# Performance work log

Measured on AMD Instinct MI355X. Metric: run time of the kernel, lower is better.

Reference implementation:

```python
import jax, jax.numpy as jnp
import numpy as np

D_MODEL, D_FF, N_EXPERTS, TOP_K = 1024, 4096, 4, 2
B, S = 4, 2048


def setup_inputs() -> dict:
    key = jax.random.key(0)
    ks = jax.random.split(key, 7)
    s_r = 1.0 / np.sqrt(D_MODEL)
    s_f = 1.0 / np.sqrt(D_FF)
    return {
        "x": jax.random.normal(ks[0], (B, S, D_MODEL), dtype=jnp.float32),
        "Wr": jax.random.uniform(ks[1], (D_MODEL, N_EXPERTS), jnp.float32, -s_r, s_r),
        "br": jnp.zeros((N_EXPERTS,), jnp.float32),
        "W1": jax.random.uniform(ks[2], (N_EXPERTS, D_MODEL, D_FF), jnp.float32, -s_r, s_r),
        "b1": jax.random.uniform(ks[3], (N_EXPERTS, D_FF), jnp.float32, -s_r, s_r),
        "W2": jax.random.uniform(ks[4], (N_EXPERTS, D_FF, D_MODEL), jnp.float32, -s_f, s_f),
        "b2": jax.random.uniform(ks[5], (N_EXPERTS, D_MODEL), jnp.float32, -s_f, s_f),
    }


def reference(x, Wr, br, W1, b1, W2, b2):
    # Router: (B,S,E)
    router_logits = jnp.einsum("bsd,de->bse", x, Wr) + br
    router_probs = jax.nn.softmax(router_logits, axis=-1)
    top_k_probs, top_k_idx = jax.lax.top_k(router_probs, TOP_K)  # (B,S,K)
    top_k_probs = top_k_probs / jnp.sum(top_k_probs, axis=-1, keepdims=True)

    # Dense all-experts compute (faithful to original module).
    h = jnp.einsum("bsd,edf->bsef", x, W1) + b1          # (B,S,E,F)
    h = jax.nn.gelu(h, approximate=False)                 # torch nn.GELU (erf)
    expert_out = jnp.einsum("bsef,efd->bsed", h, W2) + b2  # (B,S,E,D)

    # Gather top-k expert outputs and combine with renormalized probs.
    sel = jnp.take_along_axis(expert_out, top_k_idx[..., None], axis=2)  # (B,S,K,D)
    out = jnp.sum(sel * top_k_probs[..., None], axis=2)   # (B,S,D)
    return out
```

## Files before the change

### kernel.cpp

```cpp
#include <hip/hip_runtime.h>
#include <hip/hip_bf16.h>
#include <hip/hip_fp16.h>
#include <stdint.h>

typedef float    f32x4 __attribute__((ext_vector_type(4)));
typedef float    fvec4 __attribute__((ext_vector_type(4)));
typedef _Float16 f16x8 __attribute__((ext_vector_type(8)));

#define D_MODEL 1024
#define D_FF    4096
#define NTOK    8192
#define CAP_ROWS 16896
#define NRB      132

#define OFF_W1  0UL
#define OFF_W2  33554432UL
#define OFF_XG  67108864UL
#define OFF_H   101711872UL
#define OFF_CNT 240123904UL
#define OFF_CUR 240123920UL
#define OFF_OFS 240123936UL
#define OFF_TOK 240124160UL
#define OFF_WGT 240191744UL
#define OFF_E12 240259328UL
#define OFF_W12 240292096UL
#define WS_NEED 240357632UL

__device__ __forceinline__ void gload_lds16(const void* g, void* l) {
  __builtin_amdgcn_global_load_lds(
      (const __attribute__((address_space(1))) unsigned int*)g,
      (__attribute__((address_space(3))) unsigned int*)l, 16, 0, 0);
}

__device__ __forceinline__ float fast_gelu(float v) {
  float v2 = v * v;
  float y2 = v * (2.302118131f + 0.10293924f * v2);
  float t = exp2f(y2);
  return v - v * __builtin_amdgcn_rcpf(1.f + t);
}

__device__ __forceinline__ void wtrans_body(
    const float* __restrict__ in, _Float16* __restrict__ out,
    int K, int N, int e, int n0, int k0, float (*tile)[65]) {
  const float* src = in + (size_t)e * K * N;
  _Float16* dst = out + (size_t)e * K * N;
  int t = threadIdx.x;
  {
    int kk = t >> 2, nc = (t & 3) * 16;
    const float* p = src + (size_t)(k0 + kk) * N + n0 + nc;
#pragma unroll
    for (int j = 0; j < 4; ++j) {
      fvec4 v = *(const fvec4*)(p + j * 4);
      tile[kk][nc + j * 4 + 0] = v[0]; tile[kk][nc + j * 4 + 1] = v[1];
      tile[kk][nc + j * 4 + 2] = v[2]; tile[kk][nc + j * 4 + 3] = v[3];
    }
  }
  __syncthreads();
  {
    int nn = t >> 2, kb = (t & 3) * 16;
    f16x8 o0, o1;
#pragma unroll
    for (int j = 0; j < 8; ++j) o0[j] = (_Float16)tile[kb + j][nn];
#pragma unroll
    for (int j = 0; j < 8; ++j) o1[j] = (_Float16)tile[kb + 8 + j][nn];
    _Float16* q = dst + (size_t)(n0 + nn) * K + k0 + kb;
    *(f16x8*)q = o0;
    *((f16x8*)q + 1) = o1;
  }
}

__global__ __launch_bounds__(256) void rw_k(
    const float* __restrict__ x, const float* __restrict__ Wr,
    const float* __restrict__ br, int* __restrict__ e12,
    float* __restrict__ w12,
    const float* __restrict__ W1, _Float16* __restrict__ W1f) {
  __shared__ float tile[64][65];
  int b = blockIdx.x;
  if (b >= 2048) {
    int bb = b - 2048;
    int n0 = (bb & 63) * 64, k0 = ((bb >> 6) & 15) * 64, e = bb >> 10;
    wtrans_body(W1, W1f, 1024, 4096, e, n0, k0, tile);
    return;
  }
  int wid = threadIdx.x >> 6, lane = threadIdx.x & 63;
  int t = b * 4 + wid;
  const float* xr = x + (size_t)t * D_MODEL;
  float a0 = 0.f, a1 = 0.f, a2 = 0.f, a3 = 0.f;
#pragma unroll
  for (int c = 0; c < 4; ++c) {
    int d0 = c * 256 + lane * 4;
    fvec4 xv = *(const fvec4*)(xr + d0);
#pragma unroll
    for (int j = 0; j < 4; ++j) {
      fvec4 wv = *(const fvec4*)(Wr + (size_t)(d0 + j) * 4);
      a0 += xv[j] * wv[0]; a1 += xv[j] * wv[1];
      a2 += xv[j] * wv[2]; a3 += xv[j] * wv[3];
    }
  }
#pragma unroll
  for (int m = 32; m; m >>= 1) {
    a0 += __shfl_xor(a0, m, 64); a1 += __shfl_xor(a1, m, 64);
    a2 += __shfl_xor(a2, m, 64); a3 += __shfl_xor(a3, m, 64);
  }
  if (lane == 0) {
    float l[4] = {a0 + br[0], a1 + br[1], a2 + br[2], a3 + br[3]};
    int e1 = 0; float m1 = l[0];
#pragma unroll
    for (int e = 1; e < 4; ++e) if (l[e] > m1) { m1 = l[e]; e1 = e; }
    int e2 = -1; float m2 = -1e30f;
#pragma unroll
    for (int e = 0; e < 4; ++e) if (e != e1 && l[e] > m2) { m2 = l[e]; e2 = e; }
    float tt = expf(m2 - m1);
    float w1 = 1.f / (1.f + tt), w2 = tt / (1.f + tt);
    e12[t] = e1 | (e2 << 8);
    w12[2 * t] = w1; w12[2 * t + 1] = w2;
  }
}

__global__ __launch_bounds__(256) void plan_k(
    const int* __restrict__ e12, const float* __restrict__ w12,
    int* __restrict__ counts, int* __restrict__ offs,
    int* __restrict__ tok, float* __restrict__ wgt) {
  __shared__ int ls[4][256];
  __shared__ int lt[4];
  __shared__ int lo[5];
  int tid = threadIdx.x;
  int t0 = tid * 32;
  int pe[32];
  int c0 = 0, c1 = 0, c2 = 0, c3 = 0;
#pragma unroll
  for (int j = 0; j < 32; ++j) {
    int p = e12[t0 + j];
    pe[j] = p;
    int e1 = p & 255, e2 = p >> 8;
    c0 += (e1 == 0) + (e2 == 0);
    c1 += (e1 == 1) + (e2 == 1);
    c2 += (e1 == 2) + (e2 == 2);
    c3 += (e1 == 3) + (e2 == 3);
  }
  ls[0][tid] = c0; ls[1][tid] = c1; ls[2][tid] = c2; ls[3][tid] = c3;
  __syncthreads();
  int wv = tid >> 6, lane = tid & 63;
  {
    int s0 = ls[wv][lane * 4 + 0], s1 = ls[wv][lane * 4 + 1];
    int s2 = ls[wv][lane * 4 + 2], s3 = ls[wv][lane * 4 + 3];
    int s = s0 + s1 + s2 + s3;
    int incl = s;
#pragma unroll
    for (int d = 1; d < 64; d <<= 1) {
      int tsh = __shfl_up(incl, d, 64);
      if (lane >= d) incl += tsh;
    }
    int excl = incl - s;
    ls[wv][lane * 4 + 0] = excl;
    ls[wv][lane * 4 + 1] = excl + s0;
    ls[wv][lane * 4 + 2] = excl + s0 + s1;
    ls[wv][lane * 4 + 3] = excl + s0 + s1 + s2;
    if (lane == 63) lt[wv] = incl;
  }
  __syncthreads();
  if (tid == 0) {
    int o = 0;
#pragma unroll
    for (int e = 0; e < 4; ++e) {
      lo[e] = o; offs[e] = o; counts[e] = lt[e];
      o += (lt[e] + 127) & ~127;
    }
    lo[4] = o; offs[4] = o;
  }
  __syncthreads();
  int b0 = lo[0] + ls[0][tid], b1 = lo[1] + ls[1][tid];
  int b2 = lo[2] + ls[2][tid], b3 = lo[3] + ls[3][tid];
#pragma unroll
  for (int j = 0; j < 32; ++j) {
    int p = pe[j];
    int t = t0 + j;
    int e1 = p & 255, e2 = p >> 8;
    int s1 = (e1 == 0) ? b0 : (e1 == 1) ? b1 : (e1 == 2) ? b2 : b3;
    tok[s1] = t; wgt[s1] = w12[2 * t];
    b0 += (e1 == 0); b1 += (e1 == 1); b2 += (e1 == 2); b3 += (e1 == 3);
    int s2 = (e2 == 0) ? b0 : (e2 == 1) ? b1 : (e2 == 2) ? b2 : b3;
    tok[s2] = t; wgt[s2] = w12[2 * t + 1];
    b0 += (e2 == 0); b1 += (e2 == 1); b2 += (e2 == 2); b3 += (e2 == 3);
  }
}

__global__ __launch_bounds__(256) void gather_k(
    const float* __restrict__ x, const int* __restrict__ offs,
    const int* __restrict__ counts, const int* __restrict__ tok,
    _Float16* __restrict__ Xg) {
  int row = blockIdx.x * 2 + (threadIdx.x >> 7);
  int tid = threadIdx.x & 127;
  if (row >= offs[4]) return;
  int e = 0;
  while (e < 3 && row >= offs[e + 1]) ++e;
  f16x8 o;
  if (row < offs[e] + counts[e]) {
    int t = tok[row];
    const float* src = x + (size_t)t * D_MODEL + tid * 8;
    fvec4 v0 = *(const fvec4*)src;
    fvec4 v1 = *(const fvec4*)(src + 4);
#pragma unroll
    for (int j = 0; j < 4; ++j) { o[j] = (_Float16)v0[j]; o[4 + j] = (_Float16)v1[j]; }
  } else {
#pragma unroll
    for (int j = 0; j < 8; ++j) o[j] = (_Float16)0.f;
  }
  *(f16x8*)(Xg + (size_t)row * D_MODEL + tid * 8) = o;
}

__device__ __forceinline__ f16x8 lds_frag(const char* base, int row, int kbyte) {
  return *(const f16x8*)(base + row * 128 + (kbyte ^ ((row & 7) << 4)));
}

__global__ __launch_bounds__(256, 2) void gemm1x_k(
    const _Float16* __restrict__ A, const _Float16* __restrict__ B,
    const float* __restrict__ bias, const int* __restrict__ offs,
    const int* __restrict__ counts, _Float16* __restrict__ outH,
    const float* __restrict__ W2, _Float16* __restrict__ W2f,
    float* __restrict__ outz) {
  __shared__ char lds[49152];
  int bid = blockIdx.x;
  if (bid >= 6208) {
    int b2 = bid - 6208;
    fvec4 z = {0.f, 0.f, 0.f, 0.f};
#pragma unroll
    for (int j = 0; j < 4; ++j)
      *(fvec4*)(outz + (size_t)b2 * 4096 + j * 1024 + threadIdx.x * 4) = z;
    return;
  }
  if (bid >= 2112) {
    int bb = bid - 2112;
    int n0 = (bb & 15) * 64, k0 = ((bb >> 4) & 63) * 64, e = bb >> 10;
    wtrans_body(W2, W2f, 4096, 1024, e, n0, k0, (float(*)[65])lds);
    return;
  }
  int wg = (bid & 7) * 264 + (bid >> 3);
  int col = wg & 15, row = wg >> 4;
  int rowBase = row * 128;
  if (rowBase >= offs[4]) return;
  int e = 0;
  while (e < 3 && rowBase >= offs[e + 1]) ++e;
  if (rowBase >= offs[e] + counts[e]) return;
  int colBase = col * 256;

  int tid = threadIdx.x, wid = tid >> 6, lane = tid & 63;
  int wr = wid >> 1, wc = wid & 1;
  int ln = lane & 15;
  int srow = lane >> 3;
  int kx = (lane & 7) ^ srow;
  const _Float16* Abase = A + (size_t)rowBase * 1024 + kx * 8;
  const _Float16* Bbase = B + (size_t)e * D_FF * 1024 + (size_t)colBase * 1024 + kx * 8;
  char* ldsA = lds;
  char* ldsB = lds + 16384;

  f32x4 acc[4][8];
  f32x4 zero = {0.f, 0.f, 0.f, 0.f};
#pragma unroll
  for (int m = 0; m < 4; ++m)
#pragma unroll
    for (int n = 0; n < 8; ++n) acc[m][n] = zero;

  for (int k0 = 0; k0 < 1024; k0 += 64) {
#pragma unroll
    for (int i = 0; i < 4; ++i) {
      int chunk = wid * 4 + i;
      gload_lds16(Abase + (size_t)(chunk * 8 + srow) * 1024 + k0, ldsA + chunk * 1024);
    }
#pragma unroll
    for (int i = 0; i < 8; ++i) {
      int chunk = wid * 8 + i;
      gload_lds16(Bbase + (size_t)(chunk * 8 + srow) * 1024 + k0, ldsB + chunk * 1024);
    }
    __syncthreads();
#pragma unroll
    for (int kk = 0; kk < 2; ++kk) {
      int kbyte = kk * 64 + (lane >> 4) * 16;
      f16x8 af[4], bf[8];
#pragma unroll
      for (int m = 0; m < 4; ++m)
        af[m] = lds_frag(ldsA, wr * 64 + m * 16 + ln, kbyte);
#pragma unroll
      for (int n = 0; n < 8; ++n)
        bf[n] = lds_frag(ldsB, wc * 128 + n * 16 + ln, kbyte);
#pragma unroll
      for (int m = 0; m < 4; ++m)
#pragma unroll
        for (int n = 0; n < 8; ++n)
          acc[m][n] = __builtin_amdgcn_mfma_f32_16x16x32_f16(af[m], bf[n], acc[m][n], 0, 0, 0);
    }
    __syncthreads();
  }

  int col0 = colBase + wc * 128 + ln;
  float bv[8];
#pragma unroll
  for (int n = 0; n < 8; ++n) bv[n] = bias[(size_t)e * D_FF + col0 + n * 16];
#pragma unroll
  for (int m = 0; m < 4; ++m) {
    int rbase = rowBase + wr * 64 + m * 16 + (lane >> 4) * 4;
#pragma unroll
    for (int j = 0; j < 4; ++j) {
      size_t ro = (size_t)(rbase + j) * D_FF;
#pragma unroll
      for (int n = 0; n < 8; ++n) {
        float v = fast_gelu(acc[m][n][j] + bv[n]);
        outH[ro + col0 + n * 16] = (_Float16)v;
      }
    }
  }
}

__global__ __launch_bounds__(256, 3) void gemm2_k(
    const _Float16* __restrict__ A, const _Float16* __restrict__ B,
    const float* __restrict__ bias, const int* __restrict__ offs,
    const int* __restrict__ counts, const int* __restrict__ tok,
    const float* __restrict__ wgt, float* __restrict__ outF) {
  __shared__ char lds[32768];
  int bid = blockIdx.x;
  int wg = (bid & 7) * 264 + (bid >> 3);
  int col = wg & 7, kz = (wg >> 3) & 1, row = wg >> 4;
  int rowBase = row * 128;
  if (rowBase >= offs[4]) return;
  int e = 0;
  while (e < 3 && rowBase >= offs[e + 1]) ++e;
  int eoff = offs[e], cnt = counts[e];
  if (rowBase >= eoff + cnt) return;
  int colBase = col * 128;
  int kbase = kz * 2048;

  int tid = threadIdx.x, wid = tid >> 6, lane = tid & 63;
  int wr = wid >> 1, wc = wid & 1;
  int ln = lane & 15;
  int srow = lane >> 3;
  int kx = (lane & 7) ^ srow;
  const _Float16* Abase = A + (size_t)rowBase * 4096 + kx * 8;
  const _Float16* Bbase = B + (size_t)e * D_MODEL * 4096 + (size_t)colBase * 4096 + kx * 8;
  char* ldsA = lds;
  char* ldsB = lds + 16384;

  f32x4 acc[4][4];
  f32x4 zero = {0.f, 0.f, 0.f, 0.f};
#pragma unroll
  for (int m = 0; m < 4; ++m)
#pragma unroll
    for (int n = 0; n < 4; ++n) acc[m][n] = zero;

  for (int k0 = kbase; k0 < kbase + 2048; k0 += 64) {
#pragma unroll
    for (int i = 0; i < 4; ++i) {
      int chunk = wid * 4 + i;
      gload_lds16(Abase + (size_t)(chunk * 8 + srow) * 4096 + k0, ldsA + chunk * 1024);
      gload_lds16(Bbase + (size_t)(chunk * 8 + srow) * 4096 + k0, ldsB + chunk * 1024);
    }
    __syncthreads();
#pragma unroll
    for (int kk = 0; kk < 2; ++kk) {
      int kbyte = kk * 64 + (lane >> 4) * 16;
      f16x8 af[4], bf[4];
#pragma unroll
      for (int m = 0; m < 4; ++m)
        af[m] = lds_frag(ldsA, wr * 64 + m * 16 + ln, kbyte);
#pragma unroll
      for (int n = 0; n < 4; ++n)
        bf[n] = lds_frag(ldsB, wc * 64 + n * 16 + ln, kbyte);
#pragma unroll
      for (int m = 0; m < 4; ++m)
#pragma unroll
        for (int n = 0; n < 4; ++n)
          acc[m][n] = __builtin_amdgcn_mfma_f32_16x16x32_f16(af[m], bf[n], acc[m][n], 0, 0, 0);
    }
    __syncthreads();
  }

  int col0 = colBase + wc * 64 + ln;
  float bv[4];
#pragma unroll
  for (int n = 0; n < 4; ++n)
    bv[n] = (kz == 0) ? bias[(size_t)e * D_MODEL + col0 + n * 16] : 0.f;
#pragma unroll
  for (int m = 0; m < 4; ++m) {
    int rbase = rowBase + wr * 64 + m * 16 + (lane >> 4) * 4;
#pragma unroll
    for (int j = 0; j < 4; ++j) {
      int grow = rbase + j;
      if (grow - eoff < cnt) {
        int t = tok[grow];
        float w = wgt[grow];
        size_t o = (size_t)t * D_MODEL + col0;
#pragma unroll
        for (int n = 0; n < 4; ++n)
          atomicAdd(&outF[o + n * 16], w * (acc[m][n][j] + bv[n]));
      }
    }
  }
}

extern "C" void kernel_launch(void* const* d_in, const int* in_sizes, int n_in,
                              void* d_out, int out_size, void* d_ws, size_t ws_size,
                              hipStream_t stream) {
  const float* x  = (const float*)d_in[0];
  const float* Wr = (const float*)d_in[1];
  const float* br = (const float*)d_in[2];
  const float* W1 = (const float*)d_in[3];
  const float* b1 = (const float*)d_in[4];
  const float* W2 = (const float*)d_in[5];
  const float* b2 = (const float*)d_in[6];
  float* out = (float*)d_out;
  char* ws = (char*)d_ws;
  if (ws_size < WS_NEED) return;

  _Float16* W1f = (_Float16*)(ws + OFF_W1);
  _Float16* W2f = (_Float16*)(ws + OFF_W2);
  _Float16* Xg  = (_Float16*)(ws + OFF_XG);
  _Float16* H   = (_Float16*)(ws + OFF_H);
  int*   counts = (int*)(ws + OFF_CNT);
  int*   offs   = (int*)(ws + OFF_OFS);
  int*   tok    = (int*)(ws + OFF_TOK);
  float* wgt    = (float*)(ws + OFF_WGT);
  int*   e12    = (int*)(ws + OFF_E12);
  float* w12    = (float*)(ws + OFF_W12);

  rw_k<<<6144, 256, 0, stream>>>(x, Wr, br, e12, w12, W1, W1f);
  plan_k<<<1, 256, 0, stream>>>(e12, w12, counts, offs, tok, wgt);
  gather_k<<<8448, 256, 0, stream>>>(x, offs, counts, tok, Xg);
  gemm1x_k<<<8256, 256, 0, stream>>>(Xg, W1f, b1, offs, counts, H, W2, W2f, out);
  gemm2_k<<<NRB * 16, 256, 0, stream>>>(H, W2f, b2, offs, counts, tok, wgt, out);
}
```

Measured before the change: 473.8 us.

## Replace split-K atomic scatter in GEMM2 with per-slot fp16 output and combine kernel

```diff
diff --git a/kernel.cpp b/kernel.cpp
--- a/kernel.cpp
+++ b/kernel.cpp
@@ -69,21 +69,12 @@
   }
 }
 
-__global__ __launch_bounds__(256) void rw_k(
+__global__ __launch_bounds__(256) void router_k(
     const float* __restrict__ x, const float* __restrict__ Wr,
     const float* __restrict__ br, int* __restrict__ e12,
-    float* __restrict__ w12,
-    const float* __restrict__ W1, _Float16* __restrict__ W1f) {
-  __shared__ float tile[64][65];
-  int b = blockIdx.x;
-  if (b >= 2048) {
-    int bb = b - 2048;
-    int n0 = (bb & 63) * 64, k0 = ((bb >> 6) & 15) * 64, e = bb >> 10;
-    wtrans_body(W1, W1f, 1024, 4096, e, n0, k0, tile);
-    return;
-  }
+    float* __restrict__ w12) {
   int wid = threadIdx.x >> 6, lane = threadIdx.x & 63;
-  int t = b * 4 + wid;
+  int t = blockIdx.x * 4 + wid;
   const float* xr = x + (size_t)t * D_MODEL;
   float a0 = 0.f, a1 = 0.f, a2 = 0.f, a3 = 0.f;
 #pragma unroll
@@ -118,9 +109,9 @@
 }
 
 __global__ __launch_bounds__(256) void plan_k(
-    const int* __restrict__ e12, const float* __restrict__ w12,
+    int* __restrict__ e12, const float* __restrict__ w12,
     int* __restrict__ counts, int* __restrict__ offs,
-    int* __restrict__ tok, float* __restrict__ wgt) {
+    int* __restrict__ tok) {
   __shared__ int ls[4][256];
   __shared__ int lt[4];
   __shared__ int lo[5];
@@ -177,19 +168,29 @@
     int t = t0 + j;
     int e1 = p & 255, e2 = p >> 8;
     int s1 = (e1 == 0) ? b0 : (e1 == 1) ? b1 : (e1 == 2) ? b2 : b3;
-    tok[s1] = t; wgt[s1] = w12[2 * t];
+    tok[s1] = t;
     b0 += (e1 == 0); b1 += (e1 == 1); b2 += (e1 == 2); b3 += (e1 == 3);
     int s2 = (e2 == 0) ? b0 : (e2 == 1) ? b1 : (e2 == 2) ? b2 : b3;
-    tok[s2] = t; wgt[s2] = w12[2 * t + 1];
+    tok[s2] = t;
     b0 += (e2 == 0); b1 += (e2 == 1); b2 += (e2 == 2); b3 += (e2 == 3);
-  }
-}
-
-__global__ __launch_bounds__(256) void gather_k(
+    e12[t] = s1 | (s2 << 16);
+  }
+}
+
+__global__ __launch_bounds__(256) void gatherw_k(
     const float* __restrict__ x, const int* __restrict__ offs,
     const int* __restrict__ counts, const int* __restrict__ tok,
-    _Float16* __restrict__ Xg) {
-  int row = blockIdx.x * 2 + (threadIdx.x >> 7);
+    _Float16* __restrict__ Xg,
+    const float* __restrict__ W1, _Float16* __restrict__ W1f) {
+  __shared__ float tile[64][65];
+  int b = blockIdx.x;
+  if (b >= 8448) {
+    int bb = b - 8448;
+    int n0 = (bb & 63) * 64, k0 = ((bb >> 6) & 15) * 64, e = bb >> 10;
+    wtrans_body(W1, W1f, 1024, 4096, e, n0, k0, tile);
+    return;
+  }
+  int row = b * 2 + (threadIdx.x >> 7);
   int tid = threadIdx.x & 127;
   if (row >= offs[4]) return;
   int e = 0;
@@ -217,18 +218,9 @@
     const _Float16* __restrict__ A, const _Float16* __restrict__ B,
     const float* __restrict__ bias, const int* __restrict__ offs,
     const int* __restrict__ counts, _Float16* __restrict__ outH,
-    const float* __restrict__ W2, _Float16* __restrict__ W2f,
-    float* __restrict__ outz) {
+    const float* __restrict__ W2, _Float16* __restrict__ W2f) {
   __shared__ char lds[49152];
   int bid = blockIdx.x;
-  if (bid >= 6208) {
-    int b2 = bid - 6208;
-    fvec4 z = {0.f, 0.f, 0.f, 0.f};
-#pragma unroll
-    for (int j = 0; j < 4; ++j)
-      *(fvec4*)(outz + (size_t)b2 * 4096 + j * 1024 + threadIdx.x * 4) = z;
-    return;
-  }
   if (bid >= 2112) {
     int bb = bid - 2112;
     int n0 = (bb & 15) * 64, k0 = ((bb >> 4) & 63) * 64, e = bb >> 10;
@@ -311,15 +303,14 @@
   }
 }
 
-__global__ __launch_bounds__(256, 3) void gemm2_k(
+__global__ __launch_bounds__(256, 4) void gemm2_k(
     const _Float16* __restrict__ A, const _Float16* __restrict__ B,
     const float* __restrict__ bias, const int* __restrict__ offs,
-    const int* __restrict__ counts, const int* __restrict__ tok,
-    const float* __restrict__ wgt, float* __restrict__ outF) {
+    const int* __restrict__ counts, _Float16* __restrict__ Eout) {
   __shared__ char lds[32768];
   int bid = blockIdx.x;
-  int wg = (bid & 7) * 264 + (bid >> 3);
-  int col = wg & 7, kz = (wg >> 3) & 1, row = wg >> 4;
+  int wg = (bid & 7) * 132 + (bid >> 3);
+  int col = wg & 7, row = wg >> 3;
   int rowBase = row * 128;
   if (rowBase >= offs[4]) return;
   int e = 0;
@@ -327,7 +318,6 @@
   int eoff = offs[e], cnt = counts[e];
   if (rowBase >= eoff + cnt) return;
   int colBase = col * 128;
-  int kbase = kz * 2048;
 
   int tid = threadIdx.x, wid = tid >> 6, lane = tid & 63;
   int wr = wid >> 1, wc = wid & 1;
@@ -346,7 +336,7 @@
 #pragma unroll
     for (int n = 0; n < 4; ++n) acc[m][n] = zero;
 
-  for (int k0 = kbase; k0 < kbase + 2048; k0 += 64) {
+  for (int k0 = 0; k0 < 4096; k0 += 64) {
 #pragma unroll
     for (int i = 0; i < 4; ++i) {
       int chunk = wid * 4 + i;
@@ -376,8 +366,7 @@
   int col0 = colBase + wc * 64 + ln;
   float bv[4];
 #pragma unroll
-  for (int n = 0; n < 4; ++n)
-    bv[n] = (kz == 0) ? bias[(size_t)e * D_MODEL + col0 + n * 16] : 0.f;
+  for (int n = 0; n < 4; ++n) bv[n] = bias[(size_t)e * D_MODEL + col0 + n * 16];
 #pragma unroll
   for (int m = 0; m < 4; ++m) {
     int rbase = rowBase + wr * 64 + m * 16 + (lane >> 4) * 4;
@@ -385,15 +374,34 @@
     for (int j = 0; j < 4; ++j) {
       int grow = rbase + j;
       if (grow - eoff < cnt) {
-        int t = tok[grow];
-        float w = wgt[grow];
-        size_t o = (size_t)t * D_MODEL + col0;
+        size_t o = (size_t)grow * D_MODEL + col0;
 #pragma unroll
         for (int n = 0; n < 4; ++n)
-          atomicAdd(&outF[o + n * 16], w * (acc[m][n][j] + bv[n]));
+          Eout[o + n * 16] = (_Float16)(acc[m][n][j] + bv[n]);
       }
     }
   }
+}
+
+__global__ __launch_bounds__(256) void combine_k(
+    const _Float16* __restrict__ Eout, const int* __restrict__ sl12,
+    const float* __restrict__ w12, float* __restrict__ out) {
+  int t = blockIdx.x * 2 + (threadIdx.x >> 7);
+  int tid = threadIdx.x & 127;
+  int p = sl12[t];
+  int s1 = p & 0xffff, s2 = (p >> 16) & 0xffff;
+  float w1 = w12[2 * t], w2 = w12[2 * t + 1];
+  f16x8 a = *(const f16x8*)(Eout + (size_t)s1 * D_MODEL + tid * 8);
+  f16x8 b = *(const f16x8*)(Eout + (size_t)s2 * D_MODEL + tid * 8);
+  fvec4 o0, o1;
+#pragma unroll
+  for (int j = 0; j < 4; ++j) {
+    o0[j] = w1 * (float)a[j] + w2 * (float)b[j];
+    o1[j] = w1 * (float)a[4 + j] + w2 * (float)b[4 + j];
+  }
+  float* dst = out + (size_t)t * D_MODEL + tid * 8;
+  *(fvec4*)dst = o0;
+  *(fvec4*)(dst + 4) = o1;
 }
 
 extern "C" void kernel_launch(void* const* d_in, const int* in_sizes, int n_in,
@@ -417,13 +425,13 @@
   int*   counts = (int*)(ws + OFF_CNT);
   int*   offs   = (int*)(ws + OFF_OFS);
   int*   tok    = (int*)(ws + OFF_TOK);
-  float* wgt    = (float*)(ws + OFF_WGT);
   int*   e12    = (int*)(ws + OFF_E12);
   float* w12    = (float*)(ws + OFF_W12);
 
-  rw_k<<<6144, 256, 0, stream>>>(x, Wr, br, e12, w12, W1, W1f);
-  plan_k<<<1, 256, 0, stream>>>(e12, w12, counts, offs, tok, wgt);
-  gather_k<<<8448, 256, 0, stream>>>(x, offs, counts, tok, Xg);
-  gemm1x_k<<<8256, 256, 0, stream>>>(Xg, W1f, b1, offs, counts, H, W2, W2f, out);
-  gemm2_k<<<NRB * 16, 256, 0, stream>>>(H, W2f, b2, offs, counts, tok, wgt, out);
-}
+  router_k<<<NTOK / 4, 256, 0, stream>>>(x, Wr, br, e12, w12);
+  plan_k<<<1, 256, 0, stream>>>(e12, w12, counts, offs, tok);
+  gatherw_k<<<12544, 256, 0, stream>>>(x, offs, counts, tok, Xg, W1, W1f);
+  gemm1x_k<<<6208, 256, 0, stream>>>(Xg, W1f, b1, offs, counts, H, W2, W2f);
+  gemm2_k<<<NRB * 8, 256, 0, stream>>>(H, W2f, b2, offs, counts, Xg);
+  combine_k<<<NTOK / 2, 256, 0, stream>>>(Xg, e12, w12, out);
+}
```

Result: faster. 457.9 us (-3.4%).
